# Kernel optimization log

Measured on AMD Instinct MI355X. Metric: run time of the kernel, lower is better.

The kernel has to match this reference:

```python
import jax, jax.numpy as jnp
import numpy as np

NUM_CODES = 8192
LATENT_DIM = 256
BETA = 0.25
EPS_NORM = 1e-12  # F.normalize eps


def setup_inputs() -> dict:
    key = jax.random.key(0)
    k1, k2 = jax.random.split(key)
    z = jax.random.normal(k1, (8, LATENT_DIM, 32, 32), dtype=jnp.float32)
    # embedding initialized uniform(-1/K, 1/K); use that scale for realism
    codebook = jax.random.uniform(k2, (NUM_CODES, LATENT_DIM), dtype=jnp.float32,
                                  minval=-1.0 / NUM_CODES, maxval=1.0 / NUM_CODES)
    return {"z": z, "codebook": codebook}


def reference(z, codebook):
    # forward re-normalizes the codebook rows (F.normalize dim=1)
    norm = jnp.sqrt(jnp.sum(codebook * codebook, axis=1, keepdims=True))
    w = codebook / jnp.maximum(norm, EPS_NORM)                      # [K, D]

    z_perm = jnp.transpose(z, (0, 2, 3, 1))                          # [B, H, W, D]
    B, H, W, D = z_perm.shape
    zf = z_perm.reshape(-1, D)                                       # [N, D]

    # squared euclidean distances: ||z||^2 + ||w||^2 - 2 z w^T
    d = (jnp.sum(zf * zf, axis=1, keepdims=True)
         + jnp.sum(w * w, axis=1)
         - 2.0 * jnp.einsum('nd,kd->nk', zf, w))                     # [N, K]
    idx = jnp.argmin(d, axis=1)                                      # [N] int

    z_q = w[idx].reshape(B, H, W, D)                                 # gather

    # commitment + codebook loss
    loss = (jnp.mean((jax.lax.stop_gradient(z_q) - z_perm) ** 2)
            + BETA * jnp.mean((z_q - jax.lax.stop_gradient(z_perm)) ** 2))

    # straight-through estimator
    z_q = z_perm + jax.lax.stop_gradient(z_q - z_perm)

    # perplexity from codeword usage histogram (== mean of one-hots)
    N = idx.shape[0]
    counts = jnp.zeros((NUM_CODES,), dtype=jnp.float32).at[idx].add(1.0)
    avg_probs = counts / N
    perplexity = jnp.exp(-jnp.sum(avg_probs * jnp.log(avg_probs + 1e-10)))

    z_q = jnp.transpose(z_q, (0, 3, 1, 2))                           # back to NCHW
    return (z_q, idx, loss, perplexity)
```

## Files before the change

kernel.cpp:

```cpp
#include <hip/hip_runtime.h>
#include <hip/hip_bf16.h>
#include <math.h>

#define KC 8192
#define DD 256
#define NP 8192
#define ZQ_ELEMS 2097152
#define MARGIN_S 2.5e-4f
#define NPART 32

#define OFF_ABIG 0u
#define OFF_BBIG 8388608u
#define OFF_NRM  16777216u
#define OFF_WSQ  16809984u
#define OFF_PV1  16875520u
#define OFF_PV2  17924096u
#define OFF_PK1  18972672u
#define OFF_LOSSP 20021248u
#define OFF_HIST 20090880u
#define OFF_PACK 20123648u
#define OFF_LIST 20189184u
#define OFF_NFLG 20221952u

typedef __attribute__((ext_vector_type(8))) short bf16x8;
typedef __attribute__((ext_vector_type(4))) float f32x4;
typedef __attribute__((address_space(3))) void as3_void;
typedef const __attribute__((address_space(1))) void as1_cvoid;

#define GLOAD16(g, l) __builtin_amdgcn_global_load_lds((as1_cvoid*)(g), (as3_void*)(l), 16, 0, 0)

__device__ inline double waveReduceD(double v) {
#pragma unroll
    for (int off = 32; off; off >>= 1) v += __shfl_down(v, off, 64);
    return v;
}

static __device__ inline unsigned short f2bf(float f) {
    __hip_bfloat16 h = __float2bfloat16(f);
    return *(unsigned short*)&h;
}
static __device__ inline float bf2f(unsigned short u) {
    unsigned v = ((unsigned)u) << 16;
    float f;
    __builtin_memcpy(&f, &v, 4);
    return f;
}

__global__ __launch_bounds__(256) void prep(
    const float* __restrict__ cb, const float* __restrict__ z,
    unsigned short* __restrict__ Bbig, unsigned short* __restrict__ Abig,
    float* __restrict__ nrm, float* __restrict__ wsq,
    int* __restrict__ hist, int* __restrict__ nflag) {
    __shared__ float tile[64][65];
    int bid = blockIdx.x, t = threadIdx.x;
    int lane = t & 63, wid = t >> 6;
    if (bid < KC) {
        __shared__ double lred[4];
        __shared__ float mh;
        int k = bid;
        if (k < 32) hist[k * 256 + t] = 0;
        if (k == 32 && t == 0) *nflag = 0;
        float c = cb[k * DD + t];
        double s = waveReduceD((double)c * (double)c);
        if (lane == 0) lred[wid] = s;
        __syncthreads();
        if (t == 0) {
            double tot = lred[0] + lred[1] + lred[2] + lred[3];
            float nf = sqrtf((float)tot);
            mh = fmaxf(nf, 1e-12f);
            nrm[k] = mh;
            wsq[k] = (float)(tot / ((double)mh * (double)mh));
        }
        __syncthreads();
        float wv = c / mh;
        unsigned short hi = f2bf(wv);
        unsigned short lo = f2bf(wv - bf2f(hi));
        Bbig[k * 512 + t] = hi;
        Bbig[k * 512 + 256 + t] = lo;
    } else {
        int zb = bid - KC;
        int b = zb >> 6, ht = (zb >> 2) & 15, dt = zb & 3;
        int hw0 = ht * 64, d0 = dt * 64;
#pragma unroll
        for (int i = 0; i < 16; ++i) {
            int dl = wid * 16 + i;
            tile[dl][lane] = z[(size_t)(b * DD + d0 + dl) * 1024 + hw0 + lane];
        }
        __syncthreads();
#pragma unroll
        for (int i = 0; i < 16; ++i) {
            int nl = wid * 16 + i;
            float v = tile[lane][nl];
            unsigned short hi = f2bf(v);
            unsigned short lo = f2bf(v - bf2f(hi));
            size_t base = (size_t)(b * 1024 + hw0 + nl) * 512 + d0 + lane;
            Abig[base] = hi;
            Abig[base + 256] = lo;
        }
    }
}

__global__ __launch_bounds__(512, 2) void gemm_top2(
    const unsigned short* __restrict__ Abig, const unsigned short* __restrict__ Bbig,
    const float* __restrict__ wsq,
    float* __restrict__ pv1, float* __restrict__ pv2, int* __restrict__ pk1) {
    __shared__ unsigned short sAB[65536];

    int t = threadIdx.x;
    int l = t & 63, w = t >> 6;
    int wm = w >> 2, wn = w & 3;
    int kc0 = blockIdx.y * 256;
    int n0 = blockIdx.x * 256;

    int row0 = t >> 2;
    int lsw = (((t & 3) ^ ((row0 >> 1) & 3)) << 3);
    int subsw = (((l >> 4) ^ ((l >> 1) & 3)) << 3);

#define STAGE(kt_) do {                                                        \
    int p_ = (kt_) >> 3;                                                       \
    int zo_ = (p_ == 2 ? 256 : 0) + ((kt_) & 7) * 32;                          \
    int wo_ = (p_ == 1 ? 256 : 0) + ((kt_) & 7) * 32;                          \
    int b_ = ((kt_) & 3) * 16384;                                              \
    GLOAD16(Bbig + (size_t)(kc0 + row0) * 512 + wo_ + lsw, &sAB[b_ + t * 8]);  \
    GLOAD16(Bbig + (size_t)(kc0 + row0 + 128) * 512 + wo_ + lsw, &sAB[b_ + 4096 + t * 8]); \
    GLOAD16(Abig + (size_t)(n0 + row0) * 512 + zo_ + lsw, &sAB[b_ + 8192 + t * 8]); \
    GLOAD16(Abig + (size_t)(n0 + row0 + 128) * 512 + zo_ + lsw, &sAB[b_ + 12288 + t * 8]); \
} while (0)

    f32x4 acc[8][4];
#pragma unroll
    for (int mf = 0; mf < 8; ++mf) {
#pragma unroll
        for (int r = 0; r < 4; ++r) {
            float hv = -0.5f * wsq[kc0 + wm * 128 + mf * 16 + ((l >> 4) << 2) + r];
#pragma unroll
            for (int nf = 0; nf < 4; ++nf) acc[mf][nf][r] = hv;
        }
    }

#define KBODY(bufbase) do {                                                    \
    bf16x8 af[8], bfr[4];                                                      \
    _Pragma("unroll")                                                          \
    for (int mf = 0; mf < 8; ++mf)                                             \
        af[mf] = *(const bf16x8*)&sAB[(bufbase) + (wm * 128 + mf * 16 + (l & 15)) * 32 + subsw]; \
    _Pragma("unroll")                                                          \
    for (int nf = 0; nf < 4; ++nf)                                             \
        bfr[nf] = *(const bf16x8*)&sAB[(bufbase) + 8192 + (wn * 64 + nf * 16 + (l & 15)) * 32 + subsw]; \
    __builtin_amdgcn_s_setprio(1);                                             \
    _Pragma("unroll")                                                          \
    for (int mf = 0; mf < 8; ++mf)                                             \
        _Pragma("unroll")                                                      \
        for (int nf = 0; nf < 4; ++nf)                                         \
            acc[mf][nf] = __builtin_amdgcn_mfma_f32_16x16x32_bf16(af[mf], bfr[nf], acc[mf][nf], 0, 0, 0); \
    __builtin_amdgcn_s_setprio(0);                                             \
} while (0)

    STAGE(0);
    STAGE(1);
    STAGE(2);
    asm volatile("s_waitcnt vmcnt(8)" ::: "memory");
    __builtin_amdgcn_s_barrier();
    asm volatile("" ::: "memory");

    for (int kt = 0; kt < 21; ++kt) {
        STAGE(kt + 3);
        KBODY((kt & 3) * 16384);
        asm volatile("s_waitcnt vmcnt(8)" ::: "memory");
        __builtin_amdgcn_s_barrier();
        asm volatile("" ::: "memory");
    }
    KBODY(1 * 16384);
    asm volatile("s_waitcnt vmcnt(4)" ::: "memory");
    __builtin_amdgcn_s_barrier();
    asm volatile("" ::: "memory");
    KBODY(2 * 16384);
    asm volatile("s_waitcnt vmcnt(0)" ::: "memory");
    __builtin_amdgcn_s_barrier();
    asm volatile("" ::: "memory");
    KBODY(3 * 16384);

    float v1[4], v2[4];
    int k1[4];
#pragma unroll
    for (int nf = 0; nf < 4; ++nf) { v1[nf] = 3.4e38f; v2[nf] = 3.4e38f; k1[nf] = 0; }
#pragma unroll
    for (int mf = 0; mf < 8; ++mf) {
#pragma unroll
        for (int r = 0; r < 4; ++r) {
            int code = kc0 + wm * 128 + mf * 16 + ((l >> 4) << 2) + r;
#pragma unroll
            for (int nf = 0; nf < 4; ++nf) {
                float dv = -acc[mf][nf][r];
                bool lt = dv < v1[nf];
                v2[nf] = fminf(v2[nf], fmaxf(v1[nf], dv));
                v1[nf] = fminf(v1[nf], dv);
                k1[nf] = lt ? code : k1[nf];
            }
        }
    }
#pragma unroll
    for (int nf = 0; nf < 4; ++nf) {
#pragma unroll
        for (int mask = 16; mask <= 32; mask <<= 1) {
            float ov1 = __shfl_xor(v1[nf], mask, 64);
            float ov2 = __shfl_xor(v2[nf], mask, 64);
            int ok1 = __shfl_xor(k1[nf], mask, 64);
            bool take = (ov1 < v1[nf]) || (ov1 == v1[nf] && ok1 < k1[nf]);
            if (take) { v2[nf] = fminf(v1[nf], ov2); v1[nf] = ov1; k1[nf] = ok1; }
            else v2[nf] = fminf(v2[nf], ov1);
        }
    }
    __syncthreads();
    float* sv1 = (float*)sAB;
    float* sv2 = sv1 + 512;
    int* sk1 = (int*)(sv2 + 512);
    if ((l >> 4) == 0) {
#pragma unroll
        for (int nf = 0; nf < 4; ++nf) {
            int col = wn * 64 + nf * 16 + l;
            sv1[col * 2 + wm] = v1[nf];
            sv2[col * 2 + wm] = v2[nf];
            sk1[col * 2 + wm] = k1[nf];
        }
    }
    __syncthreads();
    if (t < 256) {
        float a1 = sv1[t * 2], b1 = sv1[t * 2 + 1];
        float a2 = sv2[t * 2], b2 = sv2[t * 2 + 1];
        int ak = sk1[t * 2], bk = sk1[t * 2 + 1];
        bool tb = (b1 < a1) || (b1 == a1 && bk < ak);
        float w1 = tb ? b1 : a1;
        int wk = tb ? bk : ak;
        float w2 = tb ? fminf(b2, a1) : fminf(a2, b1);
        pv1[blockIdx.y * NP + n0 + t] = w1;
        pv2[blockIdx.y * NP + n0 + t] = w2;
        pk1[blockIdx.y * NP + n0 + t] = wk;
    }
#undef STAGE
#undef KBODY
}

__global__ __launch_bounds__(256) void merge_top2(
    const float* __restrict__ pv1, const float* __restrict__ pv2,
    const int* __restrict__ pk1, int* __restrict__ list, int* __restrict__ nflag,
    unsigned long long* __restrict__ packed) {
    int n = blockIdx.x * 256 + threadIdx.x;
    float gv1 = 3.4e38f, gv2 = 3.4e38f;
    int gk1 = 0;
#pragma unroll
    for (int ct = 0; ct < NPART; ++ct) {
        float v1 = pv1[ct * NP + n];
        if (v1 < gv1) {
            gv2 = fminf(gv1, pv2[ct * NP + n]);
            gv1 = v1;
            gk1 = pk1[ct * NP + n];
        } else {
            gv2 = fminf(gv2, v1);
        }
    }
    int f = (gv2 - gv1 < MARGIN_S) ? 1 : 0;
    packed[n] = f ? 0xFFFFFFFFFFFFFFFFull : (unsigned long long)(unsigned)gk1;
    if (f) {
        int pos = atomicAdd(nflag, 1);
        list[pos] = n;
    }
}

__global__ __launch_bounds__(256) void rescore_par(
    const float* __restrict__ z, const float* __restrict__ cb,
    const float* __restrict__ nrm, const float* __restrict__ wsq,
    const int* __restrict__ list, const int* __restrict__ nflag,
    unsigned long long* __restrict__ packed) {
    __shared__ float sz[256];
    int nf = *nflag;
    int t = threadIdx.x;
    int lane = t & 63, wv = t >> 6;
    for (int ii = blockIdx.x; ii < nf; ii += 64) {
        int n = list[ii];
        int b = n >> 10, hw = n & 1023;
        __syncthreads();
        sz[t] = z[(b * DD + t) * 1024 + hw];
        __syncthreads();
        float4 zr = ((const float4*)sz)[lane];
        double zqd = (double)zr.x * zr.x + (double)zr.y * zr.y
                   + (double)zr.z * zr.z + (double)zr.w * zr.w;
#pragma unroll
        for (int off = 32; off; off >>= 1) zqd += __shfl_xor(zqd, off, 64);
        float zq = (float)zqd;
        unsigned long long best = 0xFFFFFFFFFFFFFFFFull;
        int kbase = blockIdx.y * 256 + wv * 64;
        for (int j = 0; j < 64; ++j) {
            int k = kbase + j;
            float4 cc = *(const float4*)&cb[(size_t)k * DD + lane * 4];
            float p = (zr.x * cc.x + zr.y * cc.y) + (zr.z * cc.z + zr.w * cc.w);
#pragma unroll
            for (int off = 32; off; off >>= 1) p += __shfl_xor(p, off, 64);
            float dot = p / nrm[k];
            float dv = (zq + wsq[k]) - 2.0f * dot;
            unsigned bits = __float_as_uint(dv);
            bits = (bits & 0x80000000u) ? ~bits : (bits | 0x80000000u);
            unsigned long long pk = ((unsigned long long)bits << 32) | (unsigned)k;
            best = best < pk ? best : pk;
        }
        if (lane == 0) atomicMin(packed + n, best);
    }
}

__global__ __launch_bounds__(256) void gather_loss(
    const float* __restrict__ z, const float* __restrict__ cb,
    const float* __restrict__ nrm, const unsigned long long* __restrict__ packed,
    float* __restrict__ out, double* __restrict__ lossp, int* __restrict__ hist) {
    __shared__ double lred[4];
    int t = threadIdx.x;
    int base = (blockIdx.x * 256 + t) * 16;
    double s = 0.0;
#pragma unroll
    for (int q = 0; q < 4; ++q) {
        int e = base + q * 4;
        int b = e >> 18, d = (e >> 10) & 255, hw = e & 1023;
        int n = (b << 10) + hw;
        float4 zv = *(const float4*)&z[e];
        float o[4];
        int ks[4];
#pragma unroll
        for (int j = 0; j < 4; ++j) {
            ks[j] = (int)(packed[n + j] & 0xFFFFFFFFull);
            o[j] = cb[ks[j] * DD + d] / nrm[ks[j]];
        }
        *(float4*)&out[e] = make_float4(o[0], o[1], o[2], o[3]);
        if (d == 0) {
#pragma unroll
            for (int j = 0; j < 4; ++j) {
                out[ZQ_ELEMS + n + j] = (float)ks[j];
                atomicAdd(&hist[ks[j]], 1);
            }
        }
        float d0 = o[0] - zv.x, d1 = o[1] - zv.y, d2 = o[2] - zv.z, d3 = o[3] - zv.w;
        s += (double)(d0 * d0) + (double)(d1 * d1) + (double)(d2 * d2) + (double)(d3 * d3);
    }
    s = waveReduceD(s);
    int lane = t & 63, wid = t >> 6;
    if (lane == 0) lred[wid] = s;
    __syncthreads();
    if (t == 0) lossp[blockIdx.x] = lred[0] + lred[1] + lred[2] + lred[3];
}

__global__ __launch_bounds__(256) void finalize_kernel(
    const int* __restrict__ hist, const double* __restrict__ lossp,
    float* __restrict__ out) {
    __shared__ double lred[4];
    __shared__ double lsum;
    int t = threadIdx.x;
    int lane = t & 63, wid = t >> 6;
    double ls = lossp[t] + lossp[t + 256];
    ls = waveReduceD(ls);
    if (lane == 0) lred[wid] = ls;
    __syncthreads();
    if (t == 0) lsum = lred[0] + lred[1] + lred[2] + lred[3];
    __syncthreads();
    double s = 0.0;
    for (int i = t; i < KC; i += 256) {
        float p = (float)hist[i] * (1.0f / 8192.0f);
        float lg = logf(p + 1e-10f);
        s += (double)(p * lg);
    }
    s = waveReduceD(s);
    if (lane == 0) lred[wid] = s;
    __syncthreads();
    if (t == 0) {
        double tot = lred[0] + lred[1] + lred[2] + lred[3];
        float m = (float)(lsum / (double)ZQ_ELEMS);
        out[ZQ_ELEMS + NP] = m + 0.25f * m;
        out[ZQ_ELEMS + NP + 1] = expf(-(float)tot);
    }
}

extern "C" void kernel_launch(void* const* d_in, const int* in_sizes, int n_in,
                              void* d_out, int out_size, void* d_ws, size_t ws_size,
                              hipStream_t stream) {
    const float* z = (const float*)d_in[0];
    const float* cb = (const float*)d_in[1];
    float* out = (float*)d_out;
    char* ws = (char*)d_ws;

    unsigned short* Abig = (unsigned short*)(ws + OFF_ABIG);
    unsigned short* Bbig = (unsigned short*)(ws + OFF_BBIG);
    float* nrm = (float*)(ws + OFF_NRM);
    float* wsq = (float*)(ws + OFF_WSQ);
    float* pv1 = (float*)(ws + OFF_PV1);
    float* pv2 = (float*)(ws + OFF_PV2);
    int* pk1 = (int*)(ws + OFF_PK1);
    int* hist = (int*)(ws + OFF_HIST);
    double* lossp = (double*)(ws + OFF_LOSSP);
    unsigned long long* packed = (unsigned long long*)(ws + OFF_PACK);
    int* list = (int*)(ws + OFF_LIST);
    int* nflag = (int*)(ws + OFF_NFLG);

    prep<<<KC + 512, 256, 0, stream>>>(cb, z, Bbig, Abig, nrm, wsq, hist, nflag);
    gemm_top2<<<dim3(32, NPART), 512, 0, stream>>>(Abig, Bbig, wsq, pv1, pv2, pk1);
    merge_top2<<<NP / 256, 256, 0, stream>>>(pv1, pv2, pk1, list, nflag, packed);
    rescore_par<<<dim3(64, 32), 256, 0, stream>>>(z, cb, nrm, wsq, list, nflag, packed);
    gather_loss<<<ZQ_ELEMS / (256 * 16), 256, 0, stream>>>(z, cb, nrm, packed, out, lossp, hist);
    finalize_kernel<<<1, 256, 0, stream>>>(hist, lossp, out);
}
```

Before: 208.6 us.

## Double-buffer LDS fragments in registers to overlap LDS reads with MFMA

Restructures the GEMM main loop so that the fragments for the next k-tile are read from LDS into a second register set while the current tile's MFMAs run. The loop is unrolled by two with ping-pong fragment buffers, and the barriers and waitcnts are re-sequenced. The aim is to hide LDS read latency behind matrix-core work. In exchange, register pressure roughly doubles for the fragments, which may lower occupancy or cause spills, and the reordered barriers risk LDS reuse hazards.

Measured after the change: 207.5 us. Within noise of the previous version (-0.5%).

```diff
diff --git a/kernel.cpp b/kernel.cpp
--- a/kernel.cpp
+++ b/kernel.cpp
@@ -127,57 +127,71 @@
     GLOAD16(Abig + (size_t)(n0 + row0 + 128) * 512 + zo_ + lsw, &sAB[b_ + 12288 + t * 8]); \
 } while (0)
 
-    f32x4 acc[8][4];
-#pragma unroll
-    for (int mf = 0; mf < 8; ++mf) {
-#pragma unroll
-        for (int r = 0; r < 4; ++r) {
-            float hv = -0.5f * wsq[kc0 + wm * 128 + mf * 16 + ((l >> 4) << 2) + r];
-#pragma unroll
-            for (int nf = 0; nf < 4; ++nf) acc[mf][nf][r] = hv;
-        }
-    }
-
-#define KBODY(bufbase) do {                                                    \
-    bf16x8 af[8], bfr[4];                                                      \
+#define LDFRAG(bufbase, fa, fb) do {                                           \
     _Pragma("unroll")                                                          \
     for (int mf = 0; mf < 8; ++mf)                                             \
-        af[mf] = *(const bf16x8*)&sAB[(bufbase) + (wm * 128 + mf * 16 + (l & 15)) * 32 + subsw]; \
+        fa[mf] = *(const bf16x8*)&sAB[(bufbase) + (wm * 128 + mf * 16 + (l & 15)) * 32 + subsw]; \
     _Pragma("unroll")                                                          \
     for (int nf = 0; nf < 4; ++nf)                                             \
-        bfr[nf] = *(const bf16x8*)&sAB[(bufbase) + 8192 + (wn * 64 + nf * 16 + (l & 15)) * 32 + subsw]; \
+        fb[nf] = *(const bf16x8*)&sAB[(bufbase) + 8192 + (wn * 64 + nf * 16 + (l & 15)) * 32 + subsw]; \
+} while (0)
+
+#define MFMACL(fa, fb) do {                                                    \
     __builtin_amdgcn_s_setprio(1);                                             \
     _Pragma("unroll")                                                          \
     for (int mf = 0; mf < 8; ++mf)                                             \
         _Pragma("unroll")                                                      \
         for (int nf = 0; nf < 4; ++nf)                                         \
-            acc[mf][nf] = __builtin_amdgcn_mfma_f32_16x16x32_bf16(af[mf], bfr[nf], acc[mf][nf], 0, 0, 0); \
+            acc[mf][nf] = __builtin_amdgcn_mfma_f32_16x16x32_bf16(fa[mf], fb[nf], acc[mf][nf], 0, 0, 0); \
     __builtin_amdgcn_s_setprio(0);                                             \
 } while (0)
+
+#define WAITBAR(n_) do {                                                       \
+    asm volatile("s_waitcnt vmcnt(" #n_ ")" ::: "memory");                     \
+    __builtin_amdgcn_s_barrier();                                              \
+    asm volatile("" ::: "memory");                                             \
+} while (0)
+
+    f32x4 acc[8][4];
+#pragma unroll
+    for (int mf = 0; mf < 8; ++mf) {
+#pragma unroll
+        for (int r = 0; r < 4; ++r) {
+            float hv = -0.5f * wsq[kc0 + wm * 128 + mf * 16 + ((l >> 4) << 2) + r];
+#pragma unroll
+            for (int nf = 0; nf < 4; ++nf) acc[mf][nf][r] = hv;
+        }
+    }
+
+    bf16x8 fa0[8], fb0[4], fa1[8], fb1[4];
 
     STAGE(0);
     STAGE(1);
     STAGE(2);
-    asm volatile("s_waitcnt vmcnt(8)" ::: "memory");
-    __builtin_amdgcn_s_barrier();
-    asm volatile("" ::: "memory");
-
-    for (int kt = 0; kt < 21; ++kt) {
+    WAITBAR(8);
+    LDFRAG(0, fa0, fb0);
+
+    for (int kt = 0; kt < 20; kt += 2) {
+        WAITBAR(4);
+        LDFRAG(((kt + 1) & 3) * 16384, fa1, fb1);
         STAGE(kt + 3);
-        KBODY((kt & 3) * 16384);
-        asm volatile("s_waitcnt vmcnt(8)" ::: "memory");
-        __builtin_amdgcn_s_barrier();
-        asm volatile("" ::: "memory");
-    }
-    KBODY(1 * 16384);
-    asm volatile("s_waitcnt vmcnt(4)" ::: "memory");
-    __builtin_amdgcn_s_barrier();
-    asm volatile("" ::: "memory");
-    KBODY(2 * 16384);
-    asm volatile("s_waitcnt vmcnt(0)" ::: "memory");
-    __builtin_amdgcn_s_barrier();
-    asm volatile("" ::: "memory");
-    KBODY(3 * 16384);
+        MFMACL(fa0, fb0);
+        WAITBAR(4);
+        LDFRAG(((kt + 2) & 3) * 16384, fa0, fb0);
+        STAGE(kt + 4);
+        MFMACL(fa1, fb1);
+    }
+    WAITBAR(4);
+    LDFRAG(1 * 16384, fa1, fb1);
+    STAGE(23);
+    MFMACL(fa0, fb0);
+    WAITBAR(4);
+    LDFRAG(2 * 16384, fa0, fb0);
+    MFMACL(fa1, fb1);
+    WAITBAR(0);
+    LDFRAG(3 * 16384, fa1, fb1);
+    MFMACL(fa0, fb0);
+    MFMACL(fa1, fb1);
 
     float v1[4], v2[4];
     int k1[4];
@@ -237,7 +251,9 @@
         pk1[blockIdx.y * NP + n0 + t] = wk;
     }
 #undef STAGE
-#undef KBODY
+#undef LDFRAG
+#undef MFMACL
+#undef WAITBAR
 }
 
 __global__ __launch_bounds__(256) void merge_top2(
```
